# Kernel tuning notes

Hardware: AMD Instinct MI355X
Metric: run time of the kernel (lower is better)

The kernel has to match this reference:

```python
import jax, jax.numpy as jnp
import numpy as np

D_MODEL = 768

def setup_inputs() -> dict:
    key = jax.random.key(0)
    k1, k2, k3, k4 = jax.random.split(key, 4)
    x = jax.random.normal(k1, (2, 2048, D_MODEL), dtype=jnp.float32)
    w_qkv = jax.random.normal(k2, (3 * D_MODEL, D_MODEL), dtype=jnp.float32) * (1.0 / np.sqrt(D_MODEL))
    w_fc = jax.random.normal(k3, (D_MODEL, D_MODEL), dtype=jnp.float32) * (1.0 / np.sqrt(D_MODEL))
    b_fc = jax.random.normal(k4, (D_MODEL,), dtype=jnp.float32) * 0.01
    return {"x": x, "w_qkv": w_qkv, "w_fc": w_fc, "b_fc": b_fc, "n_head": 12}


def reference(x, w_qkv, w_fc, b_fc, n_head):
    b, n, d = x.shape
    h = int(n_head)
    d_k = d // h
    temperature = float(d_k) ** 0.5  # NOTE: source MULTIPLIES by sqrt(d_k)
    qkv = x @ w_qkv.T                                  # [b, n, 3d] (qkv_bias=False)
    # rearrange 'b n (qkv d h) -> qkv b h n d' : split order is (qkv, d_k, h)
    qkv = qkv.reshape(b, n, 3, d_k, h).transpose(2, 0, 4, 1, 3)  # [3, b, h, n, d_k]
    q, k, v = qkv[0], qkv[1], qkv[2]
    attn = jnp.einsum('bhid,bhjd->bhij', q, k) * temperature      # [b, h, n, n]
    attn = jax.nn.softmax(attn, axis=-1)                           # dropout p=0 -> identity
    out = jnp.einsum('bhij,bhjd->bhid', attn, v)                   # [b, h, n, d_k]
    out = out.transpose(0, 2, 1, 3).reshape(b, n, d)               # 'b h n d -> b n (h d)'
    out = out @ w_fc.T + b_fc                                      # fc (dropout p=0 -> identity)
    return out
```

## Files before the change

kernel.cpp:

```cpp
#include <hip/hip_runtime.h>
#include <stdint.h>

typedef float f32x4 __attribute__((ext_vector_type(4)));
typedef _Float16 f16;
typedef f16 f16x8 __attribute__((ext_vector_type(8)));
typedef f16 f16x4 __attribute__((ext_vector_type(4)));

#define MFMA16(a, b, c) __builtin_amdgcn_mfma_f32_16x16x32_f16((a), (b), (c), 0, 0, 0)

typedef __attribute__((address_space(1))) const uint32_t gu32;
typedef __attribute__((address_space(3))) uint32_t lu32;
__device__ __forceinline__ void gload_lds16(const void* g, void* l) {
    __builtin_amdgcn_global_load_lds((gu32*)g, (lu32*)l, 16, 0, 0);
}

__device__ __forceinline__ size_t kv_elem(int bh, int n, int d) {
    const int kt = n >> 6, row = n & 63;
    return ((size_t)(bh * 32 + kt)) * 4096 + row * 64 + (((d >> 3) ^ (row & 7)) << 3) + (d & 7);
}

__global__ void split_inputs(const float* __restrict__ X, const float* __restrict__ Wq,
                             const float* __restrict__ Wf,
                             f16* __restrict__ Xh, f16* __restrict__ Xl,
                             f16* __restrict__ Wh, f16* __restrict__ Wfb) {
    const int tid = blockIdx.x * 256 + threadIdx.x;
    if (tid < 393216) {
        const float* s = X + (size_t)tid * 8;
        f16 hi[8], lo[8];
#pragma unroll
        for (int j = 0; j < 8; j += 4) {
            f32x4 v = *(const f32x4*)(s + j);
#pragma unroll
            for (int q = 0; q < 4; ++q) {
                f16 h = (f16)v[q];
                hi[j + q] = h;
                lo[j + q] = (f16)(v[q] - (float)h);
            }
        }
        *(f16x8*)(Xh + (size_t)tid * 8) = *(f16x8*)hi;
        *(f16x8*)(Xl + (size_t)tid * 8) = *(f16x8*)lo;
    } else if (tid < 614400) {
        const int t2 = tid - 393216;
        const int row = t2 / 96;
        const int k = (t2 % 96) * 8;
        const int c = row / 768;
        const int rem = row - c * 768;
        const int d = rem / 12;
        const int h2 = rem - d * 12;
        const int cp = c * 768 + h2 * 64 + d;
        const float* s = Wq + (size_t)row * 768 + k;
        f16 hi[8];
#pragma unroll
        for (int j = 0; j < 8; j += 4) {
            f32x4 v = *(const f32x4*)(s + j);
#pragma unroll
            for (int q = 0; q < 4; ++q) hi[j + q] = (f16)v[q];
        }
        *(f16x8*)(Wh + (size_t)cp * 768 + k) = *(f16x8*)hi;
    } else {
        const int t2 = tid - 614400;
        const float* s = Wf + (size_t)t2 * 8;
        f16 hi[8];
#pragma unroll
        for (int j = 0; j < 8; j += 4) {
            f32x4 v = *(const f32x4*)(s + j);
#pragma unroll
            for (int q = 0; q < 4; ++q) hi[j + q] = (f16)v[q];
        }
        *(f16x8*)(Wfb + (size_t)t2 * 8) = *(f16x8*)hi;
    }
}

__global__ __launch_bounds__(256) void qkv_gemm(
    const f16* __restrict__ Xh, const f16* __restrict__ Xl,
    const f16* __restrict__ Wh,
    f16* __restrict__ Qh, f16* __restrict__ Ql,
    f16* __restrict__ Khg, f16* __restrict__ Vb) {
    __shared__ f16 Ah[128 * 32], Al[128 * 32], Bh[128 * 32];
    const int t = threadIdx.x;
    const int lane = t & 63, wv = t >> 6;
    const int wm = (wv >> 1) * 64, wn = (wv & 1) * 64;
    const int r = lane & 15, g = lane >> 4;
    const int bm = blockIdx.x, bn = blockIdx.y;
    const bool full = (bn < 12);

    const int lrow = lane >> 2;
    const int lk = (lane & 3) * 8;

    f32x4 acc[4][4];
#pragma unroll
    for (int i = 0; i < 4; ++i)
#pragma unroll
        for (int j = 0; j < 4; ++j) acc[i][j] = (f32x4)0.0f;

    for (int ks = 0; ks < 768; ks += 32) {
#pragma unroll
        for (int hh = 0; hh < 2; ++hh) {
            const int ii = wv * 2 + hh;
            const int grow = ii * 16 + lrow;
            const size_t ga = (size_t)(bm * 128 + grow) * 768 + ks + lk;
            const size_t gb = (size_t)(bn * 128 + grow) * 768 + ks + lk;
            const int lbase = ii * 512;
            gload_lds16(Xh + ga, &Ah[lbase]);
            gload_lds16(Wh + gb, &Bh[lbase]);
            if (full) gload_lds16(Xl + ga, &Al[lbase]);
        }
        __syncthreads();

        f16x8 a_h[4], b[4];
#pragma unroll
        for (int mf = 0; mf < 4; ++mf) a_h[mf] = *(f16x8*)&Ah[(wm + mf * 16 + r) * 32 + g * 8];
#pragma unroll
        for (int nf = 0; nf < 4; ++nf) b[nf] = *(f16x8*)&Bh[(wn + nf * 16 + r) * 32 + g * 8];
        if (full) {
            f16x8 a_l[4];
#pragma unroll
            for (int mf = 0; mf < 4; ++mf) a_l[mf] = *(f16x8*)&Al[(wm + mf * 16 + r) * 32 + g * 8];
#pragma unroll
            for (int mf = 0; mf < 4; ++mf)
#pragma unroll
                for (int nf = 0; nf < 4; ++nf) {
                    acc[mf][nf] = MFMA16(a_h[mf], b[nf], acc[mf][nf]);
                    acc[mf][nf] = MFMA16(a_l[mf], b[nf], acc[mf][nf]);
                }
        } else {
#pragma unroll
            for (int mf = 0; mf < 4; ++mf)
#pragma unroll
                for (int nf = 0; nf < 4; ++nf)
                    acc[mf][nf] = MFMA16(a_h[mf], b[nf], acc[mf][nf]);
        }
        __syncthreads();
    }

    const int comp = bn / 6;
#pragma unroll
    for (int mf = 0; mf < 4; ++mf)
#pragma unroll
        for (int nf = 0; nf < 4; ++nf) {
            const int col = bn * 128 + wn + nf * 16 + r;
            const int h = (col >> 6) % 12;
            const int d = col & 63;
#pragma unroll
            for (int v = 0; v < 4; ++v) {
                const int row = bm * 128 + wm + mf * 16 + g * 4 + v;
                const int b2 = row >> 11, n = row & 2047;
                const int bh = b2 * 12 + h;
                float val = acc[mf][nf][v];
                if (comp == 0) {
                    const size_t dest = ((size_t)bh * 2048 + n) * 64 + d;
                    val *= 8.0f;
                    f16 hi = (f16)val;
                    Qh[dest] = hi;
                    Ql[dest] = (f16)(val - (float)hi);
                } else if (comp == 1) {
                    Khg[kv_elem(bh, n, d)] = (f16)val;
                } else {
                    Vb[((size_t)bh * 2048 + n) * 64 + d] = (f16)val;
                }
            }
        }
}

__global__ void v_transpose(const f16* __restrict__ Vb, f16* __restrict__ VTg) {
    __shared__ f16 Vt[64 * 72];
    const int t = threadIdx.x;
    const int tile = blockIdx.x;
    const f16* src = Vb + (size_t)tile * 4096;
    const int row = t >> 2, d0 = (t & 3) * 16;
    *(f16x8*)&Vt[row * 72 + d0]     = *(const f16x8*)(src + row * 64 + d0);
    *(f16x8*)&Vt[row * 72 + d0 + 8] = *(const f16x8*)(src + row * 64 + d0 + 8);
    __syncthreads();
    f16* dst = VTg + (size_t)tile * 4096;
#pragma unroll
    for (int it = 0; it < 2; ++it) {
        const int c = t + it * 256;
        const int d = c >> 3, sg = c & 7;
        const int kv0 = (sg ^ (d & 7)) * 8;
        f16 o[8];
#pragma unroll
        for (int j = 0; j < 8; ++j) o[j] = Vt[(kv0 + j) * 72 + d];
        *(f16x8*)(dst + (size_t)c * 8) = *(f16x8*)o;
    }
}

__global__ __launch_bounds__(256) void attn_kernel(
    const f16* __restrict__ Qh, const f16* __restrict__ Ql,
    const f16* __restrict__ Khg, const f16* __restrict__ VTg,
    f16* __restrict__ AO) {
    __shared__ f16 Khs[4096], VTs[4096];
    __shared__ f16 Pl[4][16 * 72];

    const int t = threadIdx.x;
    const int lane = t & 63, wv = t >> 6;
    const int r = lane & 15, g = lane >> 4;
    const int bh = blockIdx.x >> 5;
    const int qb = blockIdx.x & 31;
    const size_t headoff = (size_t)bh * 2048 * 64;
    const int q0 = qb * 64 + wv * 16;

    f16x8 qh[2], ql[2];
#pragma unroll
    for (int kc = 0; kc < 2; ++kc) {
        const size_t off = headoff + (size_t)(q0 + r) * 64 + kc * 32 + g * 8;
        qh[kc] = *(const f16x8*)(Qh + off);
        ql[kc] = *(const f16x8*)(Ql + off);
    }

    f32x4 o_acc[4];
    float m_run = -1e30f, l_run = 0.0f;
#pragma unroll
    for (int df = 0; df < 4; ++df) o_acc[df] = (f32x4)0.0f;

    for (int kt = 0; kt < 32; ++kt) {
        const size_t tb = ((size_t)bh * 32 + kt) * 4096;
#pragma unroll
        for (int c2 = 0; c2 < 2; ++c2) {
            const int c = wv * 2 + c2;
            const int go = c * 512 + lane * 8;
            gload_lds16(Khg + tb + go, &Khs[c * 512]);
            gload_lds16(VTg + tb + go, &VTs[c * 512]);
        }
        __syncthreads();

        f32x4 s[4];
#pragma unroll
        for (int cf = 0; cf < 4; ++cf) s[cf] = (f32x4)0.0f;
#pragma unroll
        for (int kc = 0; kc < 2; ++kc) {
            const int swz = (((kc * 4 + g) ^ (r & 7)) << 3);
            f16x8 ka[4];
#pragma unroll
            for (int cf = 0; cf < 4; ++cf) ka[cf] = *(f16x8*)&Khs[(cf * 16 + r) * 64 + swz];
#pragma unroll
            for (int cf = 0; cf < 4; ++cf) {
                s[cf] = MFMA16(ka[cf], qh[kc], s[cf]);
                s[cf] = MFMA16(ka[cf], ql[kc], s[cf]);
            }
        }

        float mx = -1e30f;
#pragma unroll
        for (int cf = 0; cf < 4; ++cf)
#pragma unroll
            for (int v = 0; v < 4; ++v) mx = fmaxf(mx, s[cf][v]);
        mx = fmaxf(mx, __shfl_xor(mx, 16));
        mx = fmaxf(mx, __shfl_xor(mx, 32));
        const float mn = fmaxf(m_run, mx);
        const float sc = __expf(m_run - mn);
        m_run = mn;
        float rs = 0.0f;
        f16 p16[4][4];
#pragma unroll
        for (int cf = 0; cf < 4; ++cf)
#pragma unroll
            for (int v = 0; v < 4; ++v) {
                const float p = __expf(s[cf][v] - mn);
                rs += p;
                p16[cf][v] = (f16)p;
            }
        rs += __shfl_xor(rs, 16);
        rs += __shfl_xor(rs, 32);
        l_run = l_run * sc + rs;

#pragma unroll
        for (int v = 0; v < 4; ++v) {
            const float scv = __shfl(sc, g * 4 + v);
#pragma unroll
            for (int df = 0; df < 4; ++df) o_acc[df][v] *= scv;
        }

#pragma unroll
        for (int cf = 0; cf < 4; ++cf)
            *(f16x4*)&Pl[wv][r * 72 + cf * 16 + g * 4] = *(f16x4*)p16[cf];

        asm volatile("s_waitcnt lgkmcnt(0)" ::: "memory");
        __builtin_amdgcn_sched_barrier(0);

#pragma unroll
        for (int kc = 0; kc < 2; ++kc) {
            f16x8 pa = *(f16x8*)&Pl[wv][r * 72 + kc * 32 + g * 8];
            const int swz = (((kc * 4 + g) ^ (r & 7)) << 3);
#pragma unroll
            for (int df = 0; df < 4; ++df) {
                f16x8 vb = *(f16x8*)&VTs[(df * 16 + r) * 64 + swz];
                o_acc[df] = MFMA16(pa, vb, o_acc[df]);
            }
        }
        __syncthreads();
    }

    const int bb = bh / 12, hh = bh % 12;
#pragma unroll
    for (int v = 0; v < 4; ++v) {
        const float lv = __shfl(l_run, g * 4 + v);
        const float inv = 1.0f / lv;
        const int n = q0 + g * 4 + v;
#pragma unroll
        for (int df = 0; df < 4; ++df) {
            const int col = hh * 64 + df * 16 + r;
            AO[(size_t)(bb * 2048 + n) * 768 + col] = (f16)(o_acc[df][v] * inv);
        }
    }
}

__global__ __launch_bounds__(256) void fc_gemm(const f16* __restrict__ A,
                                               const f16* __restrict__ Wfb,
                                               const float* __restrict__ bias,
                                               float* __restrict__ OUT) {
    __shared__ f16 As[128 * 72], Bs[128 * 72];
    const int t = threadIdx.x;
    const int lane = t & 63, wv = t >> 6;
    const int wm = (wv >> 1) * 64, wn = (wv & 1) * 64;
    const int r = lane & 15, g = lane >> 4;
    const int bm = blockIdx.x, bn = blockIdx.y;

    f32x4 acc[4][4];
#pragma unroll
    for (int i = 0; i < 4; ++i)
#pragma unroll
        for (int j = 0; j < 4; ++j) acc[i][j] = (f32x4)0.0f;

    for (int ks = 0; ks < 768; ks += 64) {
#pragma unroll
        for (int it = 0; it < 4; ++it) {
            const int row = (t >> 3) + it * 32;
            const int d0 = (t & 7) * 8;
            *(f16x8*)&As[row * 72 + d0] =
                *(const f16x8*)(A + (size_t)(bm * 128 + row) * 768 + ks + d0);
        }
#pragma unroll
        for (int it = 0; it < 2; ++it) {
            const int row = (t >> 2) + it * 64;
            const int k0 = (t & 3) * 16;
            const f16* wx = Wfb + (size_t)(bn * 128 + row) * 768 + ks + k0;
            *(f16x8*)&Bs[row * 72 + k0]     = *(const f16x8*)wx;
            *(f16x8*)&Bs[row * 72 + k0 + 8] = *(const f16x8*)(wx + 8);
        }
        __syncthreads();

#pragma unroll
        for (int kc = 0; kc < 2; ++kc) {
            const int koff = kc * 32 + g * 8;
            f16x8 a[4], b[4];
#pragma unroll
            for (int mf = 0; mf < 4; ++mf) a[mf] = *(f16x8*)&As[(wm + mf * 16 + r) * 72 + koff];
#pragma unroll
            for (int nf = 0; nf < 4; ++nf) b[nf] = *(f16x8*)&Bs[(wn + nf * 16 + r) * 72 + koff];
#pragma unroll
            for (int mf = 0; mf < 4; ++mf)
#pragma unroll
                for (int nf = 0; nf < 4; ++nf)
                    acc[mf][nf] = MFMA16(a[mf], b[nf], acc[mf][nf]);
        }
        __syncthreads();
    }

#pragma unroll
    for (int nf = 0; nf < 4; ++nf) {
        const int col = bn * 128 + wn + nf * 16 + r;
        const float bv = bias[col];
#pragma unroll
        for (int mf = 0; mf < 4; ++mf) {
            const int row = bm * 128 + wm + mf * 16 + g * 4;
#pragma unroll
            for (int v = 0; v < 4; ++v)
                OUT[(size_t)(row + v) * 768 + col] = acc[mf][nf][v] + bv;
        }
    }
}

extern "C" void kernel_launch(void* const* d_in, const int* in_sizes, int n_in,
                              void* d_out, int out_size, void* d_ws, size_t ws_size,
                              hipStream_t stream) {
    (void)in_sizes; (void)n_in; (void)out_size; (void)ws_size;
    const float* x     = (const float*)d_in[0];
    const float* w_qkv = (const float*)d_in[1];
    const float* w_fc  = (const float*)d_in[2];
    const float* b_fc  = (const float*)d_in[3];
    float* out = (float*)d_out;

    char* ws = (char*)d_ws;
    f16* Xh  = (f16*)ws;
    f16* Xl  = Xh + 3145728;
    f16* Qh  = Xl + 3145728;
    f16* Ql  = Qh + 3145728;
    f16* Khg = Ql + 3145728;
    f16* Vb  = Khg + 3145728;
    f16* VTg = Vb + 3145728;
    f16* AO  = VTg + 3145728;
    f16* Wh  = AO + 3145728;
    f16* Wfb = Wh + 1769472;

    split_inputs<<<2688, 256, 0, stream>>>(x, w_qkv, w_fc, Xh, Xl, Wh, Wfb);
    qkv_gemm<<<dim3(32, 18), 256, 0, stream>>>(Xh, Xl, Wh, Qh, Ql, Khg, Vb);
    v_transpose<<<768, 256, 0, stream>>>(Vb, VTg);
    attn_kernel<<<768, 256, 0, stream>>>(Qh, Ql, Khg, VTg, AO);
    fc_gemm<<<dim3(32, 6), 256, 0, stream>>>(AO, Wfb, b_fc, out);
}
```

Before: 149.4 us.

## Double-buffer LDS tiles in QKV GEMM and attention, add lazy softmax rescaling

Both the QKV GEMM and the attention kernel now keep two LDS buffers and prefetch the next K-slice or KV tile while computing on the current one, using explicit vmcnt waits and raw s_barrier in place of __syncthreads. This targets global-load latency that was previously exposed before each tile. The softmax now works in base 2, with log2(e) folded into the Q scale, so it can use exp2f. It skips the rescale of the running max and accumulator unless the max grows by more than 8, which saves exp and multiply work but lets unnormalized values grow up to 2^8 before a rescale.

```diff
diff --git a/kernel.cpp b/kernel.cpp
--- a/kernel.cpp
+++ b/kernel.cpp
@@ -7,6 +7,10 @@
 typedef f16 f16x4 __attribute__((ext_vector_type(4)));
 
 #define MFMA16(a, b, c) __builtin_amdgcn_mfma_f32_16x16x32_f16((a), (b), (c), 0, 0, 0)
+
+#define SBAR() do { __builtin_amdgcn_sched_barrier(0); \
+                    __builtin_amdgcn_s_barrier();      \
+                    __builtin_amdgcn_sched_barrier(0); } while (0)
 
 typedef __attribute__((address_space(1))) const uint32_t gu32;
 typedef __attribute__((address_space(3))) uint32_t lu32;
@@ -76,7 +80,7 @@
     const f16* __restrict__ Wh,
     f16* __restrict__ Qh, f16* __restrict__ Ql,
     f16* __restrict__ Khg, f16* __restrict__ Vb) {
-    __shared__ f16 Ah[128 * 32], Al[128 * 32], Bh[128 * 32];
+    __shared__ f16 Ah[2][4096], Al[2][4096], Bh[2][4096];
     const int t = threadIdx.x;
     const int lane = t & 63, wv = t >> 6;
     const int wm = (wv >> 1) * 64, wn = (wv & 1) * 64;
@@ -93,29 +97,40 @@
 #pragma unroll
         for (int j = 0; j < 4; ++j) acc[i][j] = (f32x4)0.0f;
 
-    for (int ks = 0; ks < 768; ks += 32) {
+    auto stage = [&](int ksi, int buf) {
 #pragma unroll
         for (int hh = 0; hh < 2; ++hh) {
             const int ii = wv * 2 + hh;
             const int grow = ii * 16 + lrow;
-            const size_t ga = (size_t)(bm * 128 + grow) * 768 + ks + lk;
-            const size_t gb = (size_t)(bn * 128 + grow) * 768 + ks + lk;
-            const int lbase = ii * 512;
-            gload_lds16(Xh + ga, &Ah[lbase]);
-            gload_lds16(Wh + gb, &Bh[lbase]);
-            if (full) gload_lds16(Xl + ga, &Al[lbase]);
-        }
-        __syncthreads();
+            const size_t ga = (size_t)(bm * 128 + grow) * 768 + ksi * 32 + lk;
+            const size_t gb = (size_t)(bn * 128 + grow) * 768 + ksi * 32 + lk;
+            gload_lds16(Xh + ga, &Ah[buf][ii * 512]);
+            gload_lds16(Wh + gb, &Bh[buf][ii * 512]);
+            if (full) gload_lds16(Xl + ga, &Al[buf][ii * 512]);
+        }
+    };
+
+    stage(0, 0);
+    int cur = 0;
+    for (int i = 0; i < 24; ++i) {
+        if (i < 23) {
+            stage(i + 1, cur ^ 1);
+            if (full) asm volatile("s_waitcnt vmcnt(6)" ::: "memory");
+            else      asm volatile("s_waitcnt vmcnt(4)" ::: "memory");
+        } else {
+            asm volatile("s_waitcnt vmcnt(0)" ::: "memory");
+        }
+        SBAR();
 
         f16x8 a_h[4], b[4];
 #pragma unroll
-        for (int mf = 0; mf < 4; ++mf) a_h[mf] = *(f16x8*)&Ah[(wm + mf * 16 + r) * 32 + g * 8];
-#pragma unroll
-        for (int nf = 0; nf < 4; ++nf) b[nf] = *(f16x8*)&Bh[(wn + nf * 16 + r) * 32 + g * 8];
+        for (int mf = 0; mf < 4; ++mf) a_h[mf] = *(f16x8*)&Ah[cur][(wm + mf * 16 + r) * 32 + g * 8];
+#pragma unroll
+        for (int nf = 0; nf < 4; ++nf) b[nf] = *(f16x8*)&Bh[cur][(wn + nf * 16 + r) * 32 + g * 8];
         if (full) {
             f16x8 a_l[4];
 #pragma unroll
-            for (int mf = 0; mf < 4; ++mf) a_l[mf] = *(f16x8*)&Al[(wm + mf * 16 + r) * 32 + g * 8];
+            for (int mf = 0; mf < 4; ++mf) a_l[mf] = *(f16x8*)&Al[cur][(wm + mf * 16 + r) * 32 + g * 8];
 #pragma unroll
             for (int mf = 0; mf < 4; ++mf)
 #pragma unroll
@@ -130,7 +145,8 @@
                 for (int nf = 0; nf < 4; ++nf)
                     acc[mf][nf] = MFMA16(a_h[mf], b[nf], acc[mf][nf]);
         }
-        __syncthreads();
+        SBAR();
+        cur ^= 1;
     }
 
     const int comp = bn / 6;
@@ -149,7 +165,7 @@
                 float val = acc[mf][nf][v];
                 if (comp == 0) {
                     const size_t dest = ((size_t)bh * 2048 + n) * 64 + d;
-                    val *= 8.0f;
+                    val *= 11.5415603372917f;
                     f16 hi = (f16)val;
                     Qh[dest] = hi;
                     Ql[dest] = (f16)(val - (float)hi);
@@ -188,7 +204,7 @@
     const f16* __restrict__ Qh, const f16* __restrict__ Ql,
     const f16* __restrict__ Khg, const f16* __restrict__ VTg,
     f16* __restrict__ AO) {
-    __shared__ f16 Khs[4096], VTs[4096];
+    __shared__ f16 Khs[2][4096], VTs[2][4096];
     __shared__ f16 Pl[4][16 * 72];
 
     const int t = threadIdx.x;
@@ -212,16 +228,27 @@
 #pragma unroll
     for (int df = 0; df < 4; ++df) o_acc[df] = (f32x4)0.0f;
 
-    for (int kt = 0; kt < 32; ++kt) {
+    auto stage = [&](int kt, int buf) {
         const size_t tb = ((size_t)bh * 32 + kt) * 4096;
 #pragma unroll
         for (int c2 = 0; c2 < 2; ++c2) {
             const int c = wv * 2 + c2;
             const int go = c * 512 + lane * 8;
-            gload_lds16(Khg + tb + go, &Khs[c * 512]);
-            gload_lds16(VTg + tb + go, &VTs[c * 512]);
-        }
-        __syncthreads();
+            gload_lds16(Khg + tb + go, &Khs[buf][c * 512]);
+            gload_lds16(VTg + tb + go, &VTs[buf][c * 512]);
+        }
+    };
+
+    stage(0, 0);
+    int cur = 0;
+    for (int kt = 0; kt < 32; ++kt) {
+        if (kt < 31) {
+            stage(kt + 1, cur ^ 1);
+            asm volatile("s_waitcnt vmcnt(4)" ::: "memory");
+        } else {
+            asm volatile("s_waitcnt vmcnt(0)" ::: "memory");
+        }
+        SBAR();
 
         f32x4 s[4];
 #pragma unroll
@@ -231,7 +258,7 @@
             const int swz = (((kc * 4 + g) ^ (r & 7)) << 3);
             f16x8 ka[4];
 #pragma unroll
-            for (int cf = 0; cf < 4; ++cf) ka[cf] = *(f16x8*)&Khs[(cf * 16 + r) * 64 + swz];
+            for (int cf = 0; cf < 4; ++cf) ka[cf] = *(f16x8*)&Khs[cur][(cf * 16 + r) * 64 + swz];
 #pragma unroll
             for (int cf = 0; cf < 4; ++cf) {
                 s[cf] = MFMA16(ka[cf], qh[kc], s[cf]);
@@ -246,29 +273,31 @@
             for (int v = 0; v < 4; ++v) mx = fmaxf(mx, s[cf][v]);
         mx = fmaxf(mx, __shfl_xor(mx, 16));
         mx = fmaxf(mx, __shfl_xor(mx, 32));
-        const float mn = fmaxf(m_run, mx);
-        const float sc = __expf(m_run - mn);
-        m_run = mn;
+        if (__any(mx - m_run > 8.0f)) {
+            const float mn = fmaxf(m_run, mx);
+            const float sc = exp2f(m_run - mn);
+            m_run = mn;
+            l_run *= sc;
+#pragma unroll
+            for (int v = 0; v < 4; ++v) {
+                const float scv = __shfl(sc, g * 4 + v);
+#pragma unroll
+                for (int df = 0; df < 4; ++df) o_acc[df][v] *= scv;
+            }
+        }
         float rs = 0.0f;
         f16 p16[4][4];
 #pragma unroll
         for (int cf = 0; cf < 4; ++cf)
 #pragma unroll
             for (int v = 0; v < 4; ++v) {
-                const float p = __expf(s[cf][v] - mn);
+                const float p = exp2f(s[cf][v] - m_run);
                 rs += p;
                 p16[cf][v] = (f16)p;
             }
         rs += __shfl_xor(rs, 16);
         rs += __shfl_xor(rs, 32);
-        l_run = l_run * sc + rs;
-
-#pragma unroll
-        for (int v = 0; v < 4; ++v) {
-            const float scv = __shfl(sc, g * 4 + v);
-#pragma unroll
-            for (int df = 0; df < 4; ++df) o_acc[df][v] *= scv;
-        }
+        l_run += rs;
 
 #pragma unroll
         for (int cf = 0; cf < 4; ++cf)
@@ -283,11 +312,12 @@
             const int swz = (((kc * 4 + g) ^ (r & 7)) << 3);
 #pragma unroll
             for (int df = 0; df < 4; ++df) {
-                f16x8 vb = *(f16x8*)&VTs[(df * 16 + r) * 64 + swz];
+                f16x8 vb = *(f16x8*)&VTs[cur][(df * 16 + r) * 64 + swz];
                 o_acc[df] = MFMA16(pa, vb, o_acc[df]);
             }
         }
-        __syncthreads();
+        SBAR();
+        cur ^= 1;
     }
 
     const int bb = bh / 12, hh = bh % 12;
```

Measured after the change: 156.9 us. 5.0% more time.

## Split attention over KV halves with combine kernel; shrink fc_gemm tiles

Applied to the files above, without the earlier changes.

Attention now splits each query block's KV range into two halves, doubling grid size, and writes unnormalized partial outputs plus running max/sum. A new combine kernel merges the two halves with log-sum-exp weights into AO. The fc GEMM moves from 128x128 tiles to 64x64 tiles with swizzled LDS to launch more blocks. The aim is better CU occupancy on the 256-CU device. The cost is an extra kernel launch, the partial-output traffic, and less per-block reuse in the GEMM.

```diff
diff --git a/kernel.cpp b/kernel.cpp
--- a/kernel.cpp
+++ b/kernel.cpp
@@ -184,18 +184,20 @@
     }
 }
 
-__global__ __launch_bounds__(256) void attn_kernel(
+__global__ __launch_bounds__(256, 6) void attn_partial(
     const f16* __restrict__ Qh, const f16* __restrict__ Ql,
     const f16* __restrict__ Khg, const f16* __restrict__ VTg,
-    f16* __restrict__ AO) {
+    f16* __restrict__ OP, float* __restrict__ Mst, float* __restrict__ Lst) {
     __shared__ f16 Khs[4096], VTs[4096];
     __shared__ f16 Pl[4][16 * 72];
 
     const int t = threadIdx.x;
     const int lane = t & 63, wv = t >> 6;
     const int r = lane & 15, g = lane >> 4;
-    const int bh = blockIdx.x >> 5;
-    const int qb = blockIdx.x & 31;
+    const int bid = blockIdx.x;
+    const int half = bid & 1;
+    const int qb = (bid >> 1) & 31;
+    const int bh = bid >> 6;
     const size_t headoff = (size_t)bh * 2048 * 64;
     const int q0 = qb * 64 + wv * 16;
 
@@ -212,7 +214,7 @@
 #pragma unroll
     for (int df = 0; df < 4; ++df) o_acc[df] = (f32x4)0.0f;
 
-    for (int kt = 0; kt < 32; ++kt) {
+    for (int kt = half * 16; kt < half * 16 + 16; ++kt) {
         const size_t tb = ((size_t)bh * 32 + kt) * 4096;
 #pragma unroll
         for (int c2 = 0; c2 < 2; ++c2) {
@@ -290,79 +292,103 @@
         __syncthreads();
     }
 
-    const int bb = bh / 12, hh = bh % 12;
-#pragma unroll
-    for (int v = 0; v < 4; ++v) {
-        const float lv = __shfl(l_run, g * 4 + v);
-        const float inv = 1.0f / lv;
-        const int n = q0 + g * 4 + v;
-#pragma unroll
-        for (int df = 0; df < 4; ++df) {
-            const int col = hh * 64 + df * 16 + r;
-            AO[(size_t)(bb * 2048 + n) * 768 + col] = (f16)(o_acc[df][v] * inv);
-        }
-    }
+    const int pb = (bh << 1) + half;
+    if (g == 0) {
+        Mst[pb * 2048 + q0 + r] = m_run;
+        Lst[pb * 2048 + q0 + r] = l_run;
+    }
+#pragma unroll
+    for (int df = 0; df < 4; ++df)
+#pragma unroll
+        for (int v = 0; v < 4; ++v) {
+            const int n = q0 + g * 4 + v;
+            OP[((size_t)pb * 2048 + n) * 64 + df * 16 + r] = (f16)o_acc[df][v];
+        }
+}
+
+__global__ void attn_combine(const f16* __restrict__ OP, const float* __restrict__ Mst,
+                             const float* __restrict__ Lst, f16* __restrict__ AO) {
+    const int tid = blockIdx.x * 256 + threadIdx.x;
+    const int d4 = (tid & 15) * 4;
+    const int pr = tid >> 4;
+    const int bh = pr >> 11, n = pr & 2047;
+    const int i1 = (bh * 2) * 2048 + n, i2 = i1 + 2048;
+    const float m1 = Mst[i1], m2 = Mst[i2];
+    const float l1 = Lst[i1], l2 = Lst[i2];
+    const float m = fmaxf(m1, m2);
+    const float w1 = __expf(m1 - m), w2 = __expf(m2 - m);
+    const float inv = 1.0f / (w1 * l1 + w2 * l2);
+    f16x4 o1 = *(const f16x4*)(OP + (size_t)i1 * 64 + d4);
+    f16x4 o2 = *(const f16x4*)(OP + (size_t)i2 * 64 + d4);
+    const int b = bh / 12, h = bh - b * 12;
+    f16 out[4];
+#pragma unroll
+    for (int j = 0; j < 4; ++j)
+        out[j] = (f16)((w1 * (float)o1[j] + w2 * (float)o2[j]) * inv);
+    *(f16x4*)(AO + ((size_t)(b * 2048 + n)) * 768 + h * 64 + d4) = *(f16x4*)out;
 }
 
 __global__ __launch_bounds__(256) void fc_gemm(const f16* __restrict__ A,
                                                const f16* __restrict__ Wfb,
                                                const float* __restrict__ bias,
                                                float* __restrict__ OUT) {
-    __shared__ f16 As[128 * 72], Bs[128 * 72];
+    __shared__ f16 As[64 * 64], Bs[64 * 64];
     const int t = threadIdx.x;
     const int lane = t & 63, wv = t >> 6;
-    const int wm = (wv >> 1) * 64, wn = (wv & 1) * 64;
+    const int wm = (wv >> 1) * 32, wn = (wv & 1) * 32;
     const int r = lane & 15, g = lane >> 4;
     const int bm = blockIdx.x, bn = blockIdx.y;
 
-    f32x4 acc[4][4];
-#pragma unroll
-    for (int i = 0; i < 4; ++i)
-#pragma unroll
-        for (int j = 0; j < 4; ++j) acc[i][j] = (f32x4)0.0f;
+    f32x4 acc[2][2];
+#pragma unroll
+    for (int i = 0; i < 2; ++i)
+#pragma unroll
+        for (int j = 0; j < 2; ++j) acc[i][j] = (f32x4)0.0f;
+
+    const int srow = t >> 2;
+    const int ssg = (t & 3) * 2;
 
     for (int ks = 0; ks < 768; ks += 64) {
-#pragma unroll
-        for (int it = 0; it < 4; ++it) {
-            const int row = (t >> 3) + it * 32;
-            const int d0 = (t & 7) * 8;
-            *(f16x8*)&As[row * 72 + d0] =
-                *(const f16x8*)(A + (size_t)(bm * 128 + row) * 768 + ks + d0);
-        }
-#pragma unroll
-        for (int it = 0; it < 2; ++it) {
-            const int row = (t >> 2) + it * 64;
-            const int k0 = (t & 3) * 16;
-            const f16* wx = Wfb + (size_t)(bn * 128 + row) * 768 + ks + k0;
-            *(f16x8*)&Bs[row * 72 + k0]     = *(const f16x8*)wx;
-            *(f16x8*)&Bs[row * 72 + k0 + 8] = *(const f16x8*)(wx + 8);
+        const f16* as = A + (size_t)(bm * 64 + srow) * 768 + ks;
+        const f16* bs = Wfb + (size_t)(bn * 64 + srow) * 768 + ks;
+#pragma unroll
+        for (int u = 0; u < 2; ++u) {
+            const int sg = ssg + u;
+            const int dst = srow * 64 + ((sg ^ (srow & 7)) << 3);
+            *(f16x8*)&As[dst] = *(const f16x8*)(as + sg * 8);
+            *(f16x8*)&Bs[dst] = *(const f16x8*)(bs + sg * 8);
         }
         __syncthreads();
 
 #pragma unroll
         for (int kc = 0; kc < 2; ++kc) {
-            const int koff = kc * 32 + g * 8;
-            f16x8 a[4], b[4];
-#pragma unroll
-            for (int mf = 0; mf < 4; ++mf) a[mf] = *(f16x8*)&As[(wm + mf * 16 + r) * 72 + koff];
-#pragma unroll
-            for (int nf = 0; nf < 4; ++nf) b[nf] = *(f16x8*)&Bs[(wn + nf * 16 + r) * 72 + koff];
-#pragma unroll
-            for (int mf = 0; mf < 4; ++mf)
-#pragma unroll
-                for (int nf = 0; nf < 4; ++nf)
+            f16x8 a[2], b[2];
+#pragma unroll
+            for (int mf = 0; mf < 2; ++mf) {
+                const int row = wm + mf * 16 + r;
+                a[mf] = *(f16x8*)&As[row * 64 + (((kc * 4 + g) ^ (row & 7)) << 3)];
+            }
+#pragma unroll
+            for (int nf = 0; nf < 2; ++nf) {
+                const int row = wn + nf * 16 + r;
+                b[nf] = *(f16x8*)&Bs[row * 64 + (((kc * 4 + g) ^ (row & 7)) << 3)];
+            }
+#pragma unroll
+            for (int mf = 0; mf < 2; ++mf)
+#pragma unroll
+                for (int nf = 0; nf < 2; ++nf)
                     acc[mf][nf] = MFMA16(a[mf], b[nf], acc[mf][nf]);
         }
         __syncthreads();
     }
 
 #pragma unroll
-    for (int nf = 0; nf < 4; ++nf) {
-        const int col = bn * 128 + wn + nf * 16 + r;
+    for (int nf = 0; nf < 2; ++nf) {
+        const int col = bn * 64 + wn + nf * 16 + r;
         const float bv = bias[col];
 #pragma unroll
-        for (int mf = 0; mf < 4; ++mf) {
-            const int row = bm * 128 + wm + mf * 16 + g * 4;
+        for (int mf = 0; mf < 2; ++mf) {
+            const int row = bm * 64 + wm + mf * 16 + g * 4;
 #pragma unroll
             for (int v = 0; v < 4; ++v)
                 OUT[(size_t)(row + v) * 768 + col] = acc[mf][nf][v] + bv;
@@ -391,10 +417,14 @@
     f16* AO  = VTg + 3145728;
     f16* Wh  = AO + 3145728;
     f16* Wfb = Wh + 1769472;
+    float* Mst = (float*)(Wfb + 589824);
+    float* Lst = Mst + 98304;
+    f16* OP = Xh;
 
     split_inputs<<<2688, 256, 0, stream>>>(x, w_qkv, w_fc, Xh, Xl, Wh, Wfb);
     qkv_gemm<<<dim3(32, 18), 256, 0, stream>>>(Xh, Xl, Wh, Qh, Ql, Khg, Vb);
     v_transpose<<<768, 256, 0, stream>>>(Vb, VTg);
-    attn_kernel<<<768, 256, 0, stream>>>(Qh, Ql, Khg, VTg, AO);
-    fc_gemm<<<dim3(32, 6), 256, 0, stream>>>(AO, Wfb, b_fc, out);
-}
+    attn_partial<<<1536, 256, 0, stream>>>(Qh, Ql, Khg, VTg, OP, Mst, Lst);
+    attn_combine<<<3072, 256, 0, stream>>>(OP, Mst, Lst, AO);
+    fc_gemm<<<dim3(64, 12), 256, 0, stream>>>(AO, Wfb, b_fc, out);
+}
```

Result: faster. 141.9 us (-5.0%).
